# Kernel tuning notes

Measured on AMD Instinct MI355X. Metric: run time of the kernel, lower is better.

## Reference

```python
import jax, jax.numpy as jnp
import numpy as np

N_NODES = 20000
N_EDGES = 640000
NODE_NF = 64
HIDDEN = 256
N_LAYERS = 4


def _linear_init(key, fan_in, fan_out, layers=None):
    shape = (fan_in, fan_out) if layers is None else (layers, fan_in, fan_out)
    scale = 1.0 / np.sqrt(fan_in)
    return jax.random.normal(key, shape, dtype=jnp.float32) * scale


def setup_inputs() -> dict:
    key = jax.random.key(0)
    ks = jax.random.split(key, 16)
    L, H = N_LAYERS, HIDDEN
    return {
        "h": jax.random.normal(ks[0], (N_NODES, NODE_NF), dtype=jnp.float32),
        "edge_index": jax.random.randint(ks[1], (2, N_EDGES), 0, N_NODES, dtype=jnp.int64),
        "coord_diff": jax.random.normal(ks[2], (N_EDGES, 3), dtype=jnp.float32),
        # embedding in / out
        "w_in": _linear_init(ks[3], NODE_NF, H),
        "b_in": jnp.zeros((H,), jnp.float32),
        "w_out": _linear_init(ks[4], H, NODE_NF),
        "b_out": jnp.zeros((NODE_NF,), jnp.float32),
        # per-layer edge MLP: Linear(2H+1 -> H), silu, Linear(H -> H), silu
        "edge_w1": _linear_init(ks[5], 2 * H + 1, H, L),
        "edge_b1": jnp.zeros((L, H), jnp.float32),
        "edge_w2": _linear_init(ks[6], H, H, L),
        "edge_b2": jnp.zeros((L, H), jnp.float32),
        # per-layer node MLP: Linear(2H -> H), silu, Linear(H -> H)
        "node_w1": _linear_init(ks[7], 2 * H, H, L),
        "node_b1": jnp.zeros((L, H), jnp.float32),
        "node_w2": _linear_init(ks[8], H, H, L),
        "node_b2": jnp.zeros((L, H), jnp.float32),
    }


def reference(h, edge_index, coord_diff, w_in, b_in, w_out, b_out,
              edge_w1, edge_b1, edge_w2, edge_b2,
              node_w1, node_b1, node_w2, node_b2):
    row, col = edge_index[0], edge_index[1]
    # radial is layer-independent: [E, 1]
    radial = jnp.sum(coord_diff ** 2, axis=1, keepdims=True)

    h = h @ w_in + b_in  # [N, H]
    n_nodes = h.shape[0]

    for l in range(N_LAYERS):
        # edge model: gather endpoints, concat with radial, 2-layer MLP
        m = jnp.concatenate([h[row], h[col], radial], axis=1)  # [E, 2H+1]
        m = jax.nn.silu(m @ edge_w1[l] + edge_b1[l])
        m = jax.nn.silu(m @ edge_w2[l] + edge_b2[l])  # [E, H]
        # node model: segment-sum aggregate over row, concat, 2-layer MLP
        agg = jax.ops.segment_sum(m, row, num_segments=n_nodes)  # [N, H]
        x = jnp.concatenate([h, agg], axis=1)  # [N, 2H]
        x = jax.nn.silu(x @ node_w1[l] + node_b1[l])
        h = x @ node_w2[l] + node_b2[l]  # recurrent=False: no residual

    return h @ w_out + b_out  # [N, node_nf]
```

## Files before the change

### kernel.cpp

```cpp
#include <hip/hip_runtime.h>
#include <hip/hip_bf16.h>
#include <cstdint>
#include <cstddef>

#define NN 20000
#define NE 640000
#define NF 64
#define HD 256
#define NL 4
#define HTS 640

typedef __attribute__((ext_vector_type(8))) short short8;
typedef __attribute__((ext_vector_type(4))) float f32x4;

__device__ __forceinline__ float bf2f(unsigned short u){
  union { unsigned int i; float f; } x; x.i = ((unsigned int)u) << 16; return x.f;
}
__device__ __forceinline__ unsigned short f2bf(float f){
  union { float f; unsigned int i; } x; x.f = f;
  unsigned int r = x.i + 0x7FFFu + ((x.i >> 16) & 1u);
  return (unsigned short)(r >> 16);
}
__device__ __forceinline__ unsigned int pk2bf(float a, float b){
  union { __hip_bfloat162 h; unsigned int u; } cv;
  cv.h = __float22bfloat162_rn(float2{a, b});
  return cv.u;
}
__device__ __forceinline__ float silu_f(float v){
  float e = __builtin_amdgcn_exp2f(v * -1.442695041f);
  return v * __builtin_amdgcn_rcpf(1.0f + e);
}
__device__ __forceinline__ void async16(const void* g, void* l){
  __builtin_amdgcn_global_load_lds(
      (const __attribute__((address_space(1))) unsigned int*)g,
      (__attribute__((address_space(3))) unsigned int*)l, 16, 0, 0);
}

__global__ __launch_bounds__(256) void prep_small(
    const float* __restrict__ w_in, const float* __restrict__ w_out,
    const float* __restrict__ ew1, const float* __restrict__ ew2,
    const float* __restrict__ nw1, const float* __restrict__ nw2,
    const float* __restrict__ eb1,
    unsigned short* __restrict__ w_in_t, unsigned short* __restrict__ w_out_t,
    unsigned short* __restrict__ ew1cat, float* __restrict__ w1r,
    float* __restrict__ b1e,
    unsigned short* __restrict__ ew2t, unsigned short* __restrict__ nw1t,
    unsigned short* __restrict__ nw2t)
{
  const int s = blockIdx.y;
  const int tid = blockIdx.x * 256 + threadIdx.x;
  if (s == 18) {
    if (tid < NL * 512) {
      int l = tid >> 9, c = tid & 511;
      b1e[tid] = (c < 256) ? eb1[l * HD + c] : 0.0f;
    }
    return;
  }
  if (s >= 2 && s < 6) {
    int l = s - 2;
    if (tid >= 513 * HD) return;
    int k = tid / HD, n = tid - k * HD;
    float v = ew1[(size_t)l * 513 * HD + tid];
    if (k == 512) { w1r[l * HD + n] = v; return; }
    unsigned short* dst = ew1cat + (size_t)l * 512 * 256;
    if (k < 256) dst[(size_t)n * 256 + k] = f2bf(v);
    else         dst[(size_t)(256 + n) * 256 + (k - 256)] = f2bf(v);
    return;
  }
  const float* src; unsigned short* dst; int K, N;
  if (s == 0)      { src = w_in;  dst = w_in_t;  K = NF;   N = HD; }
  else if (s == 1) { src = w_out; dst = w_out_t; K = HD;   N = NF; }
  else if (s < 10) { int l = s-6;  src = ew2 + (size_t)l*HD*HD;   dst = ew2t + (size_t)l*HD*HD;  K = HD;   N = HD; }
  else if (s < 14) { int l = s-10; src = nw1 + (size_t)l*2*HD*HD; dst = nw1t + (size_t)l*HD*512; K = 2*HD; N = HD; }
  else             { int l = s-14; src = nw2 + (size_t)l*HD*HD;   dst = nw2t + (size_t)l*HD*HD;  K = HD;   N = HD; }
  if (tid >= K * N) return;
  int k = tid / N, n = tid - k * N;
  dst[(size_t)n * K + k] = f2bf(src[tid]);
}

__global__ __launch_bounds__(256) void prep_big(
    const float* __restrict__ h_in, const float* __restrict__ cd,
    unsigned short* __restrict__ hb_in, float* __restrict__ radial)
{
  const int s = blockIdx.y;
  const int tid = blockIdx.x * 256 + threadIdx.x;
  if (s == 0) {
    if (tid < NN * NF) hb_in[tid] = f2bf(h_in[tid]);
  } else {
    if (tid < NE) {
      float x = cd[tid*3+0], y = cd[tid*3+1], z = cd[tid*3+2];
      radial[tid] = x*x + y*y + z*z;
    }
  }
}

__global__ __launch_bounds__(256) void hist_k(const int* __restrict__ erow, int* __restrict__ hist){
  int e = blockIdx.x * 256 + threadIdx.x;
  if (e < NE){
    unsigned r = (unsigned)erow[e]; if (r >= NN) r = 0;
    atomicAdd(&hist[r], 1);
  }
}

__global__ __launch_bounds__(256) void scan_k(const int* __restrict__ hist,
                                              int* __restrict__ starts, int* __restrict__ cursor){
  __shared__ int part[256];
  const int t = threadIdx.x;
  const int CH = 79;
  int lo = t * CH, hi = lo + CH; if (hi > NN) hi = NN; if (lo > NN) lo = NN;
  int s = 0;
  for (int i = lo; i < hi; ++i) s += hist[i];
  part[t] = s; __syncthreads();
  for (int off = 1; off < 256; off <<= 1){
    int v = (t >= off) ? part[t - off] : 0;
    __syncthreads();
    part[t] += v;
    __syncthreads();
  }
  int base = (t == 0) ? 0 : part[t - 1];
  for (int i = lo; i < hi; ++i){ starts[i] = base; cursor[i] = base; base += hist[i]; }
  if (t == 255) starts[NN] = part[255];
}

__global__ __launch_bounds__(256) void scatter_k(const int* __restrict__ erow,
                                                 int* __restrict__ cursor, int* __restrict__ sorted){
  int e = blockIdx.x * 256 + threadIdx.x;
  if (e < NE){
    unsigned r = (unsigned)erow[e]; if (r >= NN) r = 0;
    int pos = atomicAdd(&cursor[r], 1);
    sorted[pos] = e;
  }
}

__global__ __launch_bounds__(256) void gemm_k(
    const unsigned short* __restrict__ Am, const unsigned short* __restrict__ Wt,
    const float* __restrict__ bias,
    unsigned short* __restrict__ outB, float* __restrict__ outF,
    unsigned short* __restrict__ outB2,
    int M, int N, int K, int lda, int ldc, int fuseSilu)
{
  __shared__ __align__(16) unsigned short As[128*32];
  __shared__ __align__(16) unsigned short Bs[128*32];
  const int t = threadIdx.x;
  const int lane = t & 63, wave = t >> 6;
  const int ln15 = lane & 15, q = lane >> 4;
  const int bm = blockIdx.x, bn = blockIdx.y;
  const int wm = wave >> 1, wn = wave & 1;

  f32x4 acc[4][4];
  #pragma unroll
  for (int i = 0; i < 4; ++i)
    #pragma unroll
    for (int j = 0; j < 4; ++j) acc[i][j] = (f32x4){0.f,0.f,0.f,0.f};

  const int sr = t >> 2;
  const int sc = (t & 3) * 8;
  int am0 = bm*128 + sr;      if (am0 > M-1) am0 = M-1;
  int am1 = bm*128 + 64 + sr; if (am1 > M-1) am1 = M-1;
  int an0 = bn*128 + sr;      if (an0 > N-1) an0 = N-1;
  int an1 = bn*128 + 64 + sr; if (an1 > N-1) an1 = N-1;
  const unsigned short* a0 = Am + (size_t)am0 * lda + sc;
  const unsigned short* a1 = Am + (size_t)am1 * lda + sc;
  const unsigned short* b0 = Wt + (size_t)an0 * K + sc;
  const unsigned short* b1 = Wt + (size_t)an1 * K + sc;

  const int nkt = K >> 5;
  for (int kt = 0; kt < nkt; ++kt) {
    const int k0 = kt * 32;
    async16(a0 + k0, &As[t*8]);
    async16(a1 + k0, &As[2048 + t*8]);
    async16(b0 + k0, &Bs[t*8]);
    async16(b1 + k0, &Bs[2048 + t*8]);
    __syncthreads();
    short8 fa[4], fb[4];
    #pragma unroll
    for (int i = 0; i < 4; ++i)
      fa[i] = *(const short8*)&As[(wm*64 + i*16 + ln15)*32 + q*8];
    #pragma unroll
    for (int j = 0; j < 4; ++j)
      fb[j] = *(const short8*)&Bs[(wn*64 + j*16 + ln15)*32 + q*8];
    #pragma unroll
    for (int i = 0; i < 4; ++i)
      #pragma unroll
      for (int j = 0; j < 4; ++j)
        acc[i][j] = __builtin_amdgcn_mfma_f32_16x16x32_bf16(fa[i], fb[j], acc[i][j], 0, 0, 0);
    __syncthreads();
  }

  #pragma unroll
  for (int i = 0; i < 4; ++i) {
    #pragma unroll
    for (int j = 0; j < 4; ++j) {
      const int n = bn*128 + wn*64 + j*16 + ln15;
      if (n >= N) continue;
      const float bv = bias ? bias[n] : 0.0f;
      #pragma unroll
      for (int r = 0; r < 4; ++r) {
        const int m = bm*128 + wm*64 + i*16 + q*4 + r;
        if (m >= M) continue;
        float v = acc[i][j][r] + bv;
        if (fuseSilu) v = silu_f(v);
        if (outB) {
          unsigned short b = f2bf(v);
          outB[(size_t)m * ldc + n] = b;
          if (outB2 && n < 256) outB2[(size_t)m * 512 + n] = b;
        }
        else outF[(size_t)m * ldc + n] = v;
      }
    }
  }
}

__global__ __launch_bounds__(256, 4) void edge_k(
    const unsigned short* __restrict__ hT,
    const int* __restrict__ erow, const int* __restrict__ ecol,
    const float* __restrict__ radial, const int* __restrict__ sorted,
    const float* __restrict__ w1r,
    const unsigned short* __restrict__ w2t,
    const float* __restrict__ b2,
    float* __restrict__ agg)
{
  __shared__ __align__(16) unsigned short MBUF[16896];
  __shared__ float radS[64];
  __shared__ int   rowS[64];
  __shared__ float w1rS[256];
  unsigned short* M1  = MBUF;
  unsigned short* m2T = MBUF;

  const int t = threadIdx.x;
  const int lane = t & 63, wave = t >> 6;
  const int ln15 = lane & 15, q = lane >> 4;
  const int e0 = blockIdx.x * 64;
  const int sr = t >> 2;
  const int sc_swz = (((t & 3) ^ ((sr >> 1) & 3))) * 8;
  const int xq = ((q ^ ((ln15 >> 1) & 3))) * 8;

  const int es = sorted[e0 + sr];
  unsigned nr = (unsigned)erow[es]; if (nr >= NN) nr = 0;
  unsigned nc = (unsigned)ecol[es]; if (nc >= NN) nc = 0;
  const unsigned short* hr = hT + (size_t)nr * HTS + sc_swz;
  const unsigned short* hc = hT + (size_t)nc * HTS + 256 + sc_swz;
  if (t < 64) {
    int e = sorted[e0 + t];
    radS[t] = radial[e];
    unsigned r = (unsigned)erow[e]; if (r >= NN) r = 0;
    rowS[t] = (int)r;
  }
  w1rS[t] = w1r[t];

  const unsigned short* w2row[4];
  #pragma unroll
  for (int j = 0; j < 4; ++j)
    w2row[j] = w2t + (size_t)(wave*64 + j*16 + ln15) * HD + q*8;

  float bv2[4];
  #pragma unroll
  for (int j = 0; j < 4; ++j) bv2[j] = b2[wave*64 + j*16 + ln15];

  __syncthreads();
  const float rad = radS[sr];

  #pragma unroll
  for (int ch = 0; ch < 8; ++ch) {
    const int c0 = ch*32 + sc_swz;
    short8 va = *(const short8*)(hr + ch*32);
    short8 vb = *(const short8*)(hc + ch*32);
    f32x4 w0 = *(const f32x4*)&w1rS[c0];
    f32x4 w1 = *(const f32x4*)&w1rS[c0 + 4];
    const unsigned int* ua = (const unsigned int*)&va;
    const unsigned int* ub = (const unsigned int*)&vb;
    float o[8];
    #pragma unroll
    for (int i = 0; i < 4; ++i) {
      union { unsigned int i; float f; } alo, ahi, blo, bhi;
      alo.i = ua[i] << 16; ahi.i = ua[i] & 0xFFFF0000u;
      blo.i = ub[i] << 16; bhi.i = ub[i] & 0xFFFF0000u;
      o[2*i]   = alo.f + blo.f;
      o[2*i+1] = ahi.f + bhi.f;
    }
    o[0] = silu_f(o[0] + rad * w0[0]);  o[1] = silu_f(o[1] + rad * w0[1]);
    o[2] = silu_f(o[2] + rad * w0[2]);  o[3] = silu_f(o[3] + rad * w0[3]);
    o[4] = silu_f(o[4] + rad * w1[0]);  o[5] = silu_f(o[5] + rad * w1[1]);
    o[6] = silu_f(o[6] + rad * w1[2]);  o[7] = silu_f(o[7] + rad * w1[3]);
    union { unsigned int u[4]; short8 s; } res;
    res.u[0] = pk2bf(o[0], o[1]); res.u[1] = pk2bf(o[2], o[3]);
    res.u[2] = pk2bf(o[4], o[5]); res.u[3] = pk2bf(o[6], o[7]);
    *(short8*)&M1[ch*2048 + sr*32 + (t & 3)*8] = res.s;
  }
  __syncthreads();

  f32x4 acc2[4][4];
  #pragma unroll
  for (int i = 0; i < 4; ++i)
    #pragma unroll
    for (int j = 0; j < 4; ++j) acc2[i][j] = (f32x4){0.f,0.f,0.f,0.f};

  #pragma unroll
  for (int kt = 0; kt < 8; ++kt) {
    short8 fa[4], fb[4];
    #pragma unroll
    for (int j = 0; j < 4; ++j) fb[j] = *(const short8*)(w2row[j] + kt*32);
    #pragma unroll
    for (int i = 0; i < 4; ++i) fa[i] = *(const short8*)&M1[kt*2048 + (i*16 + ln15)*32 + xq];
    #pragma unroll
    for (int i = 0; i < 4; ++i)
      #pragma unroll
      for (int j = 0; j < 4; ++j)
        acc2[i][j] = __builtin_amdgcn_mfma_f32_16x16x32_bf16(fa[i], fb[j], acc2[i][j], 0, 0, 0);
  }
  __syncthreads();

  #pragma unroll
  for (int i = 0; i < 4; ++i) {
    #pragma unroll
    for (int j = 0; j < 4; ++j) {
      const int n = wave*64 + j*16 + ln15;
      f32x4 s = acc2[i][j] + bv2[j];
      float s0 = silu_f(s[0]), s1 = silu_f(s[1]), s2 = silu_f(s[2]), s3 = silu_f(s[3]);
      const int m = i*16 + q*4;
      *(unsigned int*)&m2T[n*66 + m]     = pk2bf(s0, s1);
      *(unsigned int*)&m2T[n*66 + m + 2] = pk2bf(s2, s3);
    }
  }
  __syncthreads();

  {
    const int c = t;
    int cur = __builtin_amdgcn_readfirstlane(rowS[0]);
    float s = 0.f;
    #pragma unroll
    for (int m = 0; m < 64; m += 4) {
      unsigned int u0 = *(const unsigned int*)&m2T[c*66 + m];
      unsigned int u1 = *(const unsigned int*)&m2T[c*66 + m + 2];
      int n0 = __builtin_amdgcn_readfirstlane(rowS[m]);
      int n1 = __builtin_amdgcn_readfirstlane(rowS[m+1]);
      int n2 = __builtin_amdgcn_readfirstlane(rowS[m+2]);
      int n3 = __builtin_amdgcn_readfirstlane(rowS[m+3]);
      float f0 = bf2f((unsigned short)u0), f1 = bf2f((unsigned short)(u0 >> 16));
      float f2v = bf2f((unsigned short)u1), f3 = bf2f((unsigned short)(u1 >> 16));
      if (n0 != cur) { atomicAdd(&agg[(size_t)cur * HD + c], s); s = 0.f; cur = n0; }
      s += f0;
      if (n1 != cur) { atomicAdd(&agg[(size_t)cur * HD + c], s); s = 0.f; cur = n1; }
      s += f1;
      if (n2 != cur) { atomicAdd(&agg[(size_t)cur * HD + c], s); s = 0.f; cur = n2; }
      s += f2v;
      if (n3 != cur) { atomicAdd(&agg[(size_t)cur * HD + c], s); s = 0.f; cur = n3; }
      s += f3;
    }
    atomicAdd(&agg[(size_t)cur * HD + c], s);
  }
}

__global__ __launch_bounds__(256) void aggcvt_k(
    float* __restrict__ agg, unsigned short* __restrict__ xcat)
{
  const int g = blockIdx.x * 256 + threadIdx.x;
  const int node = g >> 6;
  const int c = (g & 63) * 4;
  if (node >= NN) return;
  float4 a = *(const float4*)(agg + (size_t)node * HD + c);
  uint2 pk; pk.x = pk2bf(a.x, a.y); pk.y = pk2bf(a.z, a.w);
  *(uint2*)(xcat + (size_t)node * 2 * HD + HD + c) = pk;
  *(float4*)(agg + (size_t)node * HD + c) = float4{0.f, 0.f, 0.f, 0.f};
}

extern "C" void kernel_launch(void* const* d_in, const int* in_sizes, int n_in,
                              void* d_out, int out_size, void* d_ws, size_t ws_size,
                              hipStream_t stream)
{
  (void)in_sizes; (void)n_in; (void)out_size; (void)ws_size;
  const float* h_in  = (const float*)d_in[0];
  const int*   ei    = (const int*)d_in[1];
  const float* cd    = (const float*)d_in[2];
  const float* w_in  = (const float*)d_in[3];
  const float* b_in  = (const float*)d_in[4];
  const float* w_out = (const float*)d_in[5];
  const float* b_out = (const float*)d_in[6];
  const float* ew1   = (const float*)d_in[7];
  const float* eb1   = (const float*)d_in[8];
  const float* ew2   = (const float*)d_in[9];
  const float* eb2   = (const float*)d_in[10];
  const float* nw1   = (const float*)d_in[11];
  const float* nb1   = (const float*)d_in[12];
  const float* nw2   = (const float*)d_in[13];
  const float* nb2   = (const float*)d_in[14];
  float* out = (float*)d_out;

  char* base = (char*)d_ws;
  size_t off = 0;
  auto WS = [&](size_t bytes) -> char* {
    char* p = base + off;
    off = (off + bytes + 255) & ~(size_t)255;
    return p;
  };
  float*          radial  = (float*)WS((size_t)NE * 4);
  unsigned short* hb_in   = (unsigned short*)WS((size_t)NN * NF * 2);
  unsigned short* hcur    = (unsigned short*)WS((size_t)NN * HD * 2);
  unsigned short* xcat    = (unsigned short*)WS((size_t)NN * 2 * HD * 2);
  float*          aggF    = (float*)WS((size_t)NN * HD * 4);
  unsigned short* hT      = (unsigned short*)WS((size_t)NN * HTS * 2);
  unsigned short* x1      = hT;
  unsigned short* w_in_t  = (unsigned short*)WS((size_t)NF * HD * 2);
  unsigned short* w_out_t = (unsigned short*)WS((size_t)NF * HD * 2);
  unsigned short* ew1cat  = (unsigned short*)WS((size_t)NL * 512 * 256 * 2);
  float*          w1r     = (float*)WS((size_t)NL * HD * 4);
  float*          b1e     = (float*)WS((size_t)NL * 512 * 4);
  unsigned short* ew2t    = (unsigned short*)WS((size_t)NL * HD * HD * 2);
  unsigned short* nw1t    = (unsigned short*)WS((size_t)NL * HD * 512 * 2);
  unsigned short* nw2t    = (unsigned short*)WS((size_t)NL * HD * HD * 2);
  int*            hist    = (int*)WS((size_t)NN * 4);
  int*            starts  = (int*)WS((size_t)(NN + 1) * 4);
  int*            cursor  = (int*)WS((size_t)NN * 4);
  int*            sorted  = (int*)WS((size_t)NE * 4);

  hipMemsetAsync(hist, 0, (size_t)NN * 4, stream);
  hipMemsetAsync(aggF, 0, (size_t)NN * HD * 4, stream);
  prep_small<<<dim3(513, 19), 256, 0, stream>>>(w_in, w_out, ew1, ew2, nw1, nw2, eb1,
      w_in_t, w_out_t, ew1cat, w1r, b1e, ew2t, nw1t, nw2t);
  prep_big<<<dim3(5000, 2), 256, 0, stream>>>(h_in, cd, hb_in, radial);
  hist_k<<<NE / 256, 256, 0, stream>>>(ei, hist);
  scan_k<<<1, 256, 0, stream>>>(hist, starts, cursor);
  scatter_k<<<NE / 256, 256, 0, stream>>>(ei, cursor, sorted);

  gemm_k<<<dim3(157, 2), 256, 0, stream>>>(hb_in, w_in_t, b_in, hcur, nullptr, xcat,
      NN, HD, NF, NF, HD, 0);

  for (int l = 0; l < NL; ++l) {
    gemm_k<<<dim3(157, 4), 256, 0, stream>>>(hcur, ew1cat + (size_t)l * 512 * 256,
        b1e + (size_t)l * 512, hT, nullptr, nullptr, NN, 512, HD, HD, HTS, 0);
    edge_k<<<NE / 64, 256, 0, stream>>>(hT, ei, ei + NE, radial, sorted,
        w1r + l * HD, ew2t + (size_t)l * HD * HD, eb2 + l * HD, aggF);
    aggcvt_k<<<NN * 64 / 256, 256, 0, stream>>>(aggF, xcat);
    gemm_k<<<dim3(157, 2), 256, 0, stream>>>(xcat, nw1t + (size_t)l * HD * 512,
        nb1 + l * HD, x1, nullptr, nullptr, NN, HD, 2 * HD, 2 * HD, HD, 1);
    gemm_k<<<dim3(157, 2), 256, 0, stream>>>(x1, nw2t + (size_t)l * HD * HD,
        nb2 + l * HD, hcur, nullptr, (l < NL-1) ? xcat : nullptr, NN, HD, HD, HD, HD, 0);
  }

  gemm_k<<<dim3(157, 1), 256, 0, stream>>>(hcur, w_out_t, b_out, nullptr, out, nullptr,
      NN, NF, HD, HD, NF, 0);
}
```

Baseline: 1.364 ms.

## Bucket edges by column range, pre-gather row/col/radial, and hoist endpoint loads

Edges are now sorted by (column bucket, row) instead of row alone, so concurrently running edge blocks touch a narrower range of column nodes and get better L2 locality on the hT gathers. The sort also writes packed row/col pairs and radial values in sorted order, which removes the indirect lookups through the sorted index in edge_k. Block indices are remapped across 8 groups, presumably to spread bucket ranges across XCDs. All 16 endpoint vector loads are issued before the barrier to overlap gather latency. The cost is a 4x larger histogram and scan, plus more registers held live in edge_k.

Measured after the change: 1.488 ms. +9.1%, slower.

```diff
diff --git a/kernel.cpp b/kernel.cpp
--- a/kernel.cpp
+++ b/kernel.cpp
@@ -9,6 +9,9 @@
 #define HD 256
 #define NL 4
 #define HTS 640
+#define NBK 4
+#define BKW (NN / NBK)
+#define NBINS (NBK * NN)
 
 typedef __attribute__((ext_vector_type(8))) short short8;
 typedef __attribute__((ext_vector_type(4))) float f32x4;
@@ -94,11 +97,14 @@
   }
 }
 
-__global__ __launch_bounds__(256) void hist_k(const int* __restrict__ erow, int* __restrict__ hist){
+__global__ __launch_bounds__(256) void hist_k(const int* __restrict__ erow,
+                                              const int* __restrict__ ecol,
+                                              int* __restrict__ hist){
   int e = blockIdx.x * 256 + threadIdx.x;
   if (e < NE){
     unsigned r = (unsigned)erow[e]; if (r >= NN) r = 0;
-    atomicAdd(&hist[r], 1);
+    unsigned c = (unsigned)ecol[e]; if (c >= NN) c = 0;
+    atomicAdd(&hist[(c / BKW) * NN + r], 1);
   }
 }
 
@@ -106,8 +112,8 @@
                                               int* __restrict__ starts, int* __restrict__ cursor){
   __shared__ int part[256];
   const int t = threadIdx.x;
-  const int CH = 79;
-  int lo = t * CH, hi = lo + CH; if (hi > NN) hi = NN; if (lo > NN) lo = NN;
+  const int CH = (NBINS + 255) / 256;
+  int lo = t * CH, hi = lo + CH; if (hi > NBINS) hi = NBINS; if (lo > NBINS) lo = NBINS;
   int s = 0;
   for (int i = lo; i < hi; ++i) s += hist[i];
   part[t] = s; __syncthreads();
@@ -119,16 +125,23 @@
   }
   int base = (t == 0) ? 0 : part[t - 1];
   for (int i = lo; i < hi; ++i){ starts[i] = base; cursor[i] = base; base += hist[i]; }
-  if (t == 255) starts[NN] = part[255];
+  if (t == 255) starts[NBINS] = part[255];
 }
 
 __global__ __launch_bounds__(256) void scatter_k(const int* __restrict__ erow,
-                                                 int* __restrict__ cursor, int* __restrict__ sorted){
+                                                 const int* __restrict__ ecol,
+                                                 const float* __restrict__ radial,
+                                                 int* __restrict__ cursor,
+                                                 int* __restrict__ rowcol,
+                                                 float* __restrict__ radial_s){
   int e = blockIdx.x * 256 + threadIdx.x;
   if (e < NE){
     unsigned r = (unsigned)erow[e]; if (r >= NN) r = 0;
-    int pos = atomicAdd(&cursor[r], 1);
-    sorted[pos] = e;
+    unsigned c = (unsigned)ecol[e]; if (c >= NN) c = 0;
+    int pos = atomicAdd(&cursor[(c / BKW) * NN + r], 1);
+    rowcol[2*pos]   = (int)r;
+    rowcol[2*pos+1] = (int)c;
+    radial_s[pos] = radial[e];
   }
 }
 
@@ -213,15 +226,14 @@
 
 __global__ __launch_bounds__(256, 4) void edge_k(
     const unsigned short* __restrict__ hT,
-    const int* __restrict__ erow, const int* __restrict__ ecol,
-    const float* __restrict__ radial, const int* __restrict__ sorted,
+    const int* __restrict__ rowcol,
+    const float* __restrict__ radial_s,
     const float* __restrict__ w1r,
     const unsigned short* __restrict__ w2t,
     const float* __restrict__ b2,
     float* __restrict__ agg)
 {
   __shared__ __align__(16) unsigned short MBUF[16896];
-  __shared__ float radS[64];
   __shared__ int   rowS[64];
   __shared__ float w1rS[256];
   unsigned short* M1  = MBUF;
@@ -230,45 +242,50 @@
   const int t = threadIdx.x;
   const int lane = t & 63, wave = t >> 6;
   const int ln15 = lane & 15, q = lane >> 4;
-  const int e0 = blockIdx.x * 64;
+  int blk = blockIdx.x;
+  blk = (blk & 7) * ((int)gridDim.x >> 3) + (blk >> 3);
+  const int e0 = blk * 64;
   const int sr = t >> 2;
   const int sc_swz = (((t & 3) ^ ((sr >> 1) & 3))) * 8;
   const int xq = ((q ^ ((ln15 >> 1) & 3))) * 8;
 
-  const int es = sorted[e0 + sr];
-  unsigned nr = (unsigned)erow[es]; if (nr >= NN) nr = 0;
-  unsigned nc = (unsigned)ecol[es]; if (nc >= NN) nc = 0;
-  const unsigned short* hr = hT + (size_t)nr * HTS + sc_swz;
-  const unsigned short* hc = hT + (size_t)nc * HTS + 256 + sc_swz;
-  if (t < 64) {
-    int e = sorted[e0 + t];
-    radS[t] = radial[e];
-    unsigned r = (unsigned)erow[e]; if (r >= NN) r = 0;
-    rowS[t] = (int)r;
-  }
-  w1rS[t] = w1r[t];
+  const int2 rc = *(const int2*)(rowcol + 2*(e0 + sr));
+  int rowv = 0;
+  if (t < 64) rowv = rowcol[2*(e0 + t)];
+  const float w1v = w1r[t];
+  const float rad = radial_s[e0 + sr];
+
+  float bv2[4];
+  #pragma unroll
+  for (int j = 0; j < 4; ++j) bv2[j] = b2[wave*64 + j*16 + ln15];
+
+  const unsigned short* hr = hT + (size_t)rc.x * HTS + sc_swz;
+  const unsigned short* hc = hT + (size_t)rc.y * HTS + 256 + sc_swz;
+
+  short8 va[8], vb[8];
+  #pragma unroll
+  for (int ch = 0; ch < 8; ++ch) {
+    va[ch] = *(const short8*)(hr + ch*32);
+    vb[ch] = *(const short8*)(hc + ch*32);
+  }
+
+  if (t < 64) rowS[t] = rowv;
+  w1rS[t] = w1v;
 
   const unsigned short* w2row[4];
   #pragma unroll
   for (int j = 0; j < 4; ++j)
     w2row[j] = w2t + (size_t)(wave*64 + j*16 + ln15) * HD + q*8;
 
-  float bv2[4];
-  #pragma unroll
-  for (int j = 0; j < 4; ++j) bv2[j] = b2[wave*64 + j*16 + ln15];
-
   __syncthreads();
-  const float rad = radS[sr];
 
   #pragma unroll
   for (int ch = 0; ch < 8; ++ch) {
     const int c0 = ch*32 + sc_swz;
-    short8 va = *(const short8*)(hr + ch*32);
-    short8 vb = *(const short8*)(hc + ch*32);
     f32x4 w0 = *(const f32x4*)&w1rS[c0];
     f32x4 w1 = *(const f32x4*)&w1rS[c0 + 4];
-    const unsigned int* ua = (const unsigned int*)&va;
-    const unsigned int* ub = (const unsigned int*)&vb;
+    const unsigned int* ua = (const unsigned int*)&va[ch];
+    const unsigned int* ub = (const unsigned int*)&vb[ch];
     float o[8];
     #pragma unroll
     for (int i = 0; i < 4; ++i) {
@@ -408,19 +425,20 @@
   unsigned short* ew2t    = (unsigned short*)WS((size_t)NL * HD * HD * 2);
   unsigned short* nw1t    = (unsigned short*)WS((size_t)NL * HD * 512 * 2);
   unsigned short* nw2t    = (unsigned short*)WS((size_t)NL * HD * HD * 2);
-  int*            hist    = (int*)WS((size_t)NN * 4);
-  int*            starts  = (int*)WS((size_t)(NN + 1) * 4);
-  int*            cursor  = (int*)WS((size_t)NN * 4);
-  int*            sorted  = (int*)WS((size_t)NE * 4);
-
-  hipMemsetAsync(hist, 0, (size_t)NN * 4, stream);
+  int*            hist    = (int*)WS((size_t)NBINS * 4);
+  int*            starts  = (int*)WS((size_t)(NBINS + 1) * 4);
+  int*            cursor  = (int*)WS((size_t)NBINS * 4);
+  int*            rowcol  = (int*)WS((size_t)NE * 2 * 4);
+  float*          radial_s= (float*)WS((size_t)NE * 4);
+
+  hipMemsetAsync(hist, 0, (size_t)NBINS * 4, stream);
   hipMemsetAsync(aggF, 0, (size_t)NN * HD * 4, stream);
   prep_small<<<dim3(513, 19), 256, 0, stream>>>(w_in, w_out, ew1, ew2, nw1, nw2, eb1,
       w_in_t, w_out_t, ew1cat, w1r, b1e, ew2t, nw1t, nw2t);
   prep_big<<<dim3(5000, 2), 256, 0, stream>>>(h_in, cd, hb_in, radial);
-  hist_k<<<NE / 256, 256, 0, stream>>>(ei, hist);
+  hist_k<<<NE / 256, 256, 0, stream>>>(ei, ei + NE, hist);
   scan_k<<<1, 256, 0, stream>>>(hist, starts, cursor);
-  scatter_k<<<NE / 256, 256, 0, stream>>>(ei, cursor, sorted);
+  scatter_k<<<NE / 256, 256, 0, stream>>>(ei, ei + NE, radial, cursor, rowcol, radial_s);
 
   gemm_k<<<dim3(157, 2), 256, 0, stream>>>(hb_in, w_in_t, b_in, hcur, nullptr, xcat,
       NN, HD, NF, NF, HD, 0);
@@ -428,7 +446,7 @@
   for (int l = 0; l < NL; ++l) {
     gemm_k<<<dim3(157, 4), 256, 0, stream>>>(hcur, ew1cat + (size_t)l * 512 * 256,
         b1e + (size_t)l * 512, hT, nullptr, nullptr, NN, 512, HD, HD, HTS, 0);
-    edge_k<<<NE / 64, 256, 0, stream>>>(hT, ei, ei + NE, radial, sorted,
+    edge_k<<<NE / 64, 256, 0, stream>>>(hT, rowcol, radial_s,
         w1r + l * HD, ew2t + (size_t)l * HD * HD, eb2 + l * HD, aggF);
     aggcvt_k<<<NN * 64 / 256, 256, 0, stream>>>(aggF, xcat);
     gemm_k<<<dim3(157, 2), 256, 0, stream>>>(xcat, nw1t + (size_t)l * HD * 512,
```
